# Kernel tuning notes

Measured on AMD Instinct MI355X. Metric: run time of the kernel, lower is better.

Reference implementation:

```python
import math
import jax, jax.numpy as jnp
import numpy as np

S, B, IN, D, H, L, F, WIN = 500, 32, 256, 512, 8, 2, 2048, 100


def setup_inputs() -> dict:
    key = jax.random.key(0)
    ks = jax.random.split(key, 20)
    s = 0.02
    inp = {
        "x": jax.random.normal(ks[0], (S, B, IN), dtype=jnp.float32),
        "W_emb": jax.random.normal(ks[1], (IN, D), dtype=jnp.float32) * s,
        "b_emb": jnp.zeros((D,), jnp.float32),
        "Wq": jax.random.normal(ks[2], (L, D, D), dtype=jnp.float32) * s,
        "bq": jnp.zeros((L, D), jnp.float32),
        "Wk": jax.random.normal(ks[3], (L, D, D), dtype=jnp.float32) * s,
        "bk": jnp.zeros((L, D), jnp.float32),
        "Wv": jax.random.normal(ks[4], (L, D, D), dtype=jnp.float32) * s,
        "bv": jnp.zeros((L, D), jnp.float32),
        "Wo": jax.random.normal(ks[5], (L, D, D), dtype=jnp.float32) * s,
        "bo": jnp.zeros((L, D), jnp.float32),
        "ln1_s": jnp.ones((L, D), jnp.float32),
        "ln1_b": jnp.zeros((L, D), jnp.float32),
        "W1": jax.random.normal(ks[6], (L, D, F), dtype=jnp.float32) * s,
        "b1": jnp.zeros((L, F), jnp.float32),
        "W2": jax.random.normal(ks[7], (L, F, D), dtype=jnp.float32) * s,
        "b2": jnp.zeros((L, D), jnp.float32),
        "ln2_s": jnp.ones((L, D), jnp.float32),
        "ln2_b": jnp.zeros((L, D), jnp.float32),
    }
    return inp


def _pos_encoding(seq_len, d_model, dtype):
    pos = jnp.arange(seq_len, dtype=dtype)[:, None]
    div = jnp.exp(jnp.arange(0, d_model, 2, dtype=dtype) * (-math.log(10000.0) / d_model))
    ang = pos * div  # [S, D/2]
    # interleave sin/cos -> pe[:,0::2]=sin, pe[:,1::2]=cos
    return jnp.stack([jnp.sin(ang), jnp.cos(ang)], axis=-1).reshape(seq_len, d_model)


def _layernorm(y, scale, bias, eps=1e-5):
    m = y.mean(-1, keepdims=True)
    v = ((y - m) ** 2).mean(-1, keepdims=True)
    return (y - m) / jnp.sqrt(v + eps) * scale + bias


def reference(x, W_emb, b_emb, Wq, bq, Wk, bk, Wv, bv, Wo, bo,
              ln1_s, ln1_b, W1, b1, W2, b2, ln2_s, ln2_b):
    seq_len, batch, _ = x.shape
    d_model = W_emb.shape[1]
    n_layers = Wq.shape[0]
    hd = d_model // H

    # embedding + positional encoding (dropout is identity in eval mode)
    h = x @ W_emb + b_emb + _pos_encoding(seq_len, d_model, x.dtype)[:, None, :]

    idx = jnp.arange(seq_len)
    diff = idx[:, None] - idx[None, :]
    amask = jnp.where((diff >= 0) & (diff < WIN), 0.0, -jnp.inf).astype(x.dtype)

    for l in range(n_layers):
        # multi-head self-attention (post-norm encoder layer)
        q = (h @ Wq[l] + bq[l]).reshape(seq_len, batch, H, hd)
        k = (h @ Wk[l] + bk[l]).reshape(seq_len, batch, H, hd)
        v = (h @ Wv[l] + bv[l]).reshape(seq_len, batch, H, hd)
        scores = jnp.einsum('ibhd,jbhd->bhij', q, k) / math.sqrt(hd) + amask
        attn = jax.nn.softmax(scores, axis=-1)
        o = jnp.einsum('bhij,jbhd->ibhd', attn, v).reshape(seq_len, batch, d_model)
        h = _layernorm(h + o @ Wo[l] + bo[l], ln1_s[l], ln1_b[l])
        # feed-forward (relu)
        ff = jax.nn.relu(h @ W1[l] + b1[l]) @ W2[l] + b2[l]
        h = _layernorm(h + ff, ln2_s[l], ln2_b[l])
    return h
```

## Files before the change

### kernel.cpp

```cpp
#include <hip/hip_runtime.h>
#include <stdint.h>

#define SEQ   500
#define BATCH 32
#define DIN   256
#define DM    512
#define NH    8
#define NL    2
#define DF    2048
#define WINSZ 100
#define HD    64
#define ROWS  (SEQ*BATCH)
#define MPAD  16128

typedef __bf16 bf16x8 __attribute__((ext_vector_type(8)));
typedef float  f32x4  __attribute__((ext_vector_type(4)));

__device__ __forceinline__ unsigned short bfbits(float f) {
    unsigned int u = __builtin_bit_cast(unsigned int, f);
    u = u + 0x7fffu + ((u >> 16) & 1u);
    return (unsigned short)(u >> 16);
}
__device__ __forceinline__ unsigned int pack2(float a, float b) {
    return (unsigned int)bfbits(a) | ((unsigned int)bfbits(b) << 16);
}
__device__ __forceinline__ float blo(unsigned int u) { return __builtin_bit_cast(float, u << 16); }
__device__ __forceinline__ float bhi(unsigned int u) { return __builtin_bit_cast(float, u & 0xffff0000u); }

__device__ __forceinline__ void async16(void* lds, const void* g) {
    __builtin_amdgcn_global_load_lds((__attribute__((address_space(1))) void*)(void*)g,
                                     (__attribute__((address_space(3))) void*)(void*)lds,
                                     16, 0, 0);
}

__global__ __launch_bounds__(256) void tcast_k(const float* __restrict__ src,
                                               unsigned short* __restrict__ dst,
                                               int R, int C) {
    __shared__ float t[32][33];
    int c0 = blockIdx.x * 32, r0 = blockIdx.y * 32;
    int tx = threadIdx.x, ty = threadIdx.y;
#pragma unroll
    for (int k = 0; k < 32; k += 8)
        t[ty + k][tx] = src[(size_t)(r0 + ty + k) * C + c0 + tx];
    __syncthreads();
#pragma unroll
    for (int k = 0; k < 32; k += 8)
        dst[(size_t)(c0 + ty + k) * R + r0 + tx] = bfbits(t[tx][ty + k]);
}

__global__ __launch_bounds__(256) void prep_k(const float* __restrict__ bq,
                                              const float* __restrict__ bk,
                                              const float* __restrict__ bv,
                                              float* __restrict__ bias_qkv,
                                              float* __restrict__ pe) {
    int tid = blockIdx.x * 256 + threadIdx.x;
    if (tid < SEQ * DM) {
        int s = tid >> 9, c = tid & 511;
        int p = c >> 1;
        float div = expf(-(float)(2 * p) * (9.210340371976184f / 512.0f));
        float ang = (float)s * div;
        pe[tid] = (c & 1) ? cosf(ang) : sinf(ang);
    }
    if (tid < NL * 3 * DM) {
        int l = tid / (3 * DM), r = tid % (3 * DM);
        float v = (r < DM) ? bq[l * DM + r]
                : (r < 2 * DM) ? bk[l * DM + r - DM]
                               : bv[l * DM + r - 2 * DM];
        bias_qkv[tid] = v;
    }
}

__global__ __launch_bounds__(256) void xcast_k(const float* __restrict__ x,
                                               unsigned short* __restrict__ xb, int n) {
    int i = (blockIdx.x * 256 + threadIdx.x) * 4;
    if (i < n) {
        float4 v = *(const float4*)&x[i];
        uint2 o; o.x = pack2(v.x, v.y); o.y = pack2(v.z, v.w);
        *(uint2*)&xb[i] = o;
    }
}

template <int MODE>
__global__ __launch_bounds__(256) void gemm_k(const unsigned short* __restrict__ A,
                                              const unsigned short* __restrict__ Wt,
                                              const float* __restrict__ bias,
                                              float* __restrict__ outF,
                                              unsigned short* __restrict__ outB,
                                              const float* __restrict__ pe,
                                              int M, int N, int K) {
    __shared__ unsigned short As[128 * 32];
    __shared__ unsigned short Bs[128 * 32];
    const int tid = threadIdx.x;
    const int lane = tid & 63, wid = tid >> 6;
    const int wr = wid >> 1, wc = wid & 1;
    const int m0 = blockIdx.x * 128, n0 = blockIdx.y * 128;
    const int lr = lane & 15, kg = (lane >> 4) * 8;

    f32x4 acc[4][4] = {};

    for (int k0 = 0; k0 < K; k0 += 32) {
#pragma unroll
        for (int r = 0; r < 2; ++r) {
            int chunk = r * 256 + tid;
            int row = chunk >> 2;
            int kc  = (chunk & 3) << 3;
            async16(&As[chunk * 8], A  + (size_t)(m0 + row) * K + k0 + kc);
            async16(&Bs[chunk * 8], Wt + (size_t)(n0 + row) * K + k0 + kc);
        }
        __syncthreads();
        bf16x8 af[4], bf[4];
#pragma unroll
        for (int f = 0; f < 4; ++f) {
            af[f] = *(const bf16x8*)&As[(wr * 64 + f * 16 + lr) * 32 + kg];
            bf[f] = *(const bf16x8*)&Bs[(wc * 64 + f * 16 + lr) * 32 + kg];
        }
#pragma unroll
        for (int i = 0; i < 4; ++i)
#pragma unroll
            for (int j = 0; j < 4; ++j)
                acc[i][j] = __builtin_amdgcn_mfma_f32_16x16x32_bf16(af[i], bf[j], acc[i][j], 0, 0, 0);
        __syncthreads();
    }

#pragma unroll
    for (int i = 0; i < 4; ++i) {
#pragma unroll
        for (int j = 0; j < 4; ++j) {
            int col = n0 + wc * 64 + j * 16 + lr;
            float bv = bias[col];
#pragma unroll
            for (int v = 0; v < 4; ++v) {
                int row = m0 + wr * 64 + i * 16 + (lane >> 4) * 4 + v;
                float val = acc[i][j][v] + bv;
                size_t idx = (size_t)row * N + col;
                if (MODE == 0) {
                    outF[idx] = val;
                } else if (MODE == 1) {
                    outB[idx] = bfbits(val);
                } else if (MODE == 2) {
                    outB[idx] = bfbits(fmaxf(val, 0.f));
                } else {
                    float t = val + pe[(size_t)(row >> 5) * DM + col];
                    outF[idx] = t;
                    outB[idx] = bfbits(t);
                }
            }
        }
    }
}

template <int BM, int BN, int MODE>
__global__ __launch_bounds__((BM == 256 ? 512 : 256), 2)
void gemm2_k(const unsigned short* __restrict__ A,
             const unsigned short* __restrict__ Wt,
             const float* __restrict__ bias,
             unsigned short* __restrict__ outB,
             int Mt, int Nt, int K, int N) {
    constexpr int NTH = (BM == 256) ? 512 : 256;
    constexpr int NWC = BN / 64;
    constexpr int NWR = (NTH / 64) / NWC;
    constexpr int MI  = BM / (NWR * 16);
    constexpr int MIH = (MI > 4) ? MI / 2 : MI;
    constexpr int JSH = (BN == 256) ? 6 : 5;

    __shared__ unsigned short LA[4][BM * 32];
    __shared__ unsigned short LB[4][BN * 32];

    const int tid = threadIdx.x, lane = tid & 63, wid = tid >> 6;
    const int wr = wid / NWC, wc = wid % NWC;
    const int lr = lane & 15, grp = lane >> 4;

    int lin = blockIdx.x;
    int base_m = (lin / (8 * Nt)) * 8;
    int Gc = min(8, Mt - base_m);
    int rem = lin - base_m * Nt;
    int mt = base_m + rem % Gc, nt = rem / Gc;
    const int m0 = mt * BM, n0 = nt * BN;

    const int NKT = K >> 5;

    auto stageA = [&](int kt, int part) {
        int slot = kt & 3, k0 = kt << 5;
        int g = part * NTH + tid;
        int row = g >> 2, c = g & 3;
        int src = c ^ ((row >> 1) & 3);
        async16(&LA[slot][g * 8], A + (size_t)(m0 + row) * K + k0 + src * 8);
    };
    auto stageB = [&](int kt, int part) {
        int slot = kt & 3, k0 = kt << 5;
        int g = part * NTH + tid;
        int pos = g >> 2, cs = g & 3;
        int j   = pos >> JSH;
        int wcc = (pos >> 4) & (NWC - 1);
        int lrr = pos & 15;
        int rb  = wcc * 64 + lrr * 4 + j;
        int c   = cs ^ ((rb >> 3) & 3);
        async16(&LB[slot][g * 8], Wt + (size_t)(n0 + rb) * K + k0 + c * 8);
    };

    f32x4 acc[MI][4] = {};

#pragma unroll
    for (int t = 0; t < 3; ++t) {
        stageA(t, 0); stageA(t, 1); stageB(t, 0); stageB(t, 1);
    }

    for (int kt = 0; kt < NKT; ++kt) {
        const int slot = kt & 3;
        const bool pf = (kt + 3 < NKT);
        if (kt + 2 < NKT)      asm volatile("s_waitcnt vmcnt(8)" ::: "memory");
        else if (kt + 1 < NKT) asm volatile("s_waitcnt vmcnt(4)" ::: "memory");
        else                   asm volatile("s_waitcnt vmcnt(0)" ::: "memory");
        __builtin_amdgcn_s_barrier();
        __builtin_amdgcn_sched_barrier(0);

        const int bxor = grp ^ ((lr >> 1) & 3);
        bf16x8 af[MI], bf[4];

#pragma unroll
        for (int i = 0; i < MIH; ++i) {
            int ra = wr * (MI * 16) + i * 16 + lr;
            af[i] = *(const bf16x8*)&LA[slot][ra * 32 + ((grp ^ ((ra >> 1) & 3)) << 3)];
        }
#pragma unroll
        for (int j = 0; j < 2; ++j) {
            int pos = j * (16 * NWC) + wc * 16 + lr;
            bf[j] = *(const bf16x8*)&LB[slot][(pos * 4 + bxor) * 8];
        }
        if (pf) { stageA(kt + 3, 0); if (MI == 4) stageA(kt + 3, 1); }
        __builtin_amdgcn_s_setprio(1);
#pragma unroll
        for (int i = 0; i < MIH; ++i)
#pragma unroll
            for (int j = 0; j < 2; ++j)
                acc[i][j] = __builtin_amdgcn_mfma_f32_16x16x32_bf16(af[i], bf[j], acc[i][j], 0, 0, 0);
        __builtin_amdgcn_s_setprio(0);
        __builtin_amdgcn_s_barrier();
        __builtin_amdgcn_sched_barrier(0);

#pragma unroll
        for (int j = 2; j < 4; ++j) {
            int pos = j * (16 * NWC) + wc * 16 + lr;
            bf[j] = *(const bf16x8*)&LB[slot][(pos * 4 + bxor) * 8];
        }
        if (pf) { if (MI == 4) { stageB(kt + 3, 0); stageB(kt + 3, 1); } else stageA(kt + 3, 1); }
        __builtin_amdgcn_s_setprio(1);
#pragma unroll
        for (int i = 0; i < MIH; ++i)
#pragma unroll
            for (int j = 2; j < 4; ++j)
                acc[i][j] = __builtin_amdgcn_mfma_f32_16x16x32_bf16(af[i], bf[j], acc[i][j], 0, 0, 0);
        __builtin_amdgcn_s_setprio(0);
        __builtin_amdgcn_s_barrier();
        __builtin_amdgcn_sched_barrier(0);

        if constexpr (MI > 4) {
#pragma unroll
            for (int i = MIH; i < MI; ++i) {
                int ra = wr * (MI * 16) + i * 16 + lr;
                af[i] = *(const bf16x8*)&LA[slot][ra * 32 + ((grp ^ ((ra >> 1) & 3)) << 3)];
            }
            if (pf) stageB(kt + 3, 0);
            __builtin_amdgcn_s_setprio(1);
#pragma unroll
            for (int i = MIH; i < MI; ++i)
#pragma unroll
                for (int j = 0; j < 2; ++j)
                    acc[i][j] = __builtin_amdgcn_mfma_f32_16x16x32_bf16(af[i], bf[j], acc[i][j], 0, 0, 0);
            __builtin_amdgcn_s_setprio(0);
            __builtin_amdgcn_s_barrier();
            __builtin_amdgcn_sched_barrier(0);

            if (pf) stageB(kt + 3, 1);
            __builtin_amdgcn_s_setprio(1);
#pragma unroll
            for (int i = MIH; i < MI; ++i)
#pragma unroll
                for (int j = 2; j < 4; ++j)
                    acc[i][j] = __builtin_amdgcn_mfma_f32_16x16x32_bf16(af[i], bf[j], acc[i][j], 0, 0, 0);
            __builtin_amdgcn_s_setprio(0);
            __builtin_amdgcn_s_barrier();
            __builtin_amdgcn_sched_barrier(0);
        }
    }

    const int colb = n0 + wc * 64 + lr * 4;
    float4 bv4 = *(const float4*)&bias[colb];
#pragma unroll
    for (int i = 0; i < MI; ++i) {
#pragma unroll
        for (int v = 0; v < 4; ++v) {
            int row = m0 + wr * (MI * 16) + i * 16 + grp * 4 + v;
            float f0 = acc[i][0][v] + bv4.x;
            float f1 = acc[i][1][v] + bv4.y;
            float f2 = acc[i][2][v] + bv4.z;
            float f3 = acc[i][3][v] + bv4.w;
            if (MODE == 2) {
                f0 = fmaxf(f0, 0.f); f1 = fmaxf(f1, 0.f);
                f2 = fmaxf(f2, 0.f); f3 = fmaxf(f3, 0.f);
            }
            uint2 wv; wv.x = pack2(f0, f1); wv.y = pack2(f2, f3);
            *(uint2*)&outB[(size_t)row * N + colb] = wv;
        }
    }
}

__global__ __launch_bounds__(256) void vtrans_k(const unsigned short* __restrict__ qkv,
                                                unsigned short* __restrict__ vT) {
    __shared__ unsigned short t[32][72];
    const int s0 = blockIdx.x * 32;
    const int bh = blockIdx.y;
    const int b = bh >> 3, h = bh & 7;
    const int tid = threadIdx.x;
    {
        int sl = tid >> 3;
        int c  = tid & 7;
        int s  = s0 + sl;
        uint4 val = {0, 0, 0, 0};
        if (s < SEQ)
            val = *(const uint4*)&qkv[(size_t)(s * BATCH + b) * (3 * DM) + 2 * DM + h * HD + c * 8];
        *(uint4*)&t[sl][c * 8] = val;
    }
    __syncthreads();
    {
        int d  = tid >> 2;
        int s8 = (tid & 3) * 8;
        unsigned short v[8];
#pragma unroll
        for (int j = 0; j < 8; ++j) v[j] = t[s8 + j][d];
        *(uint4*)&vT[(size_t)(bh * 64 + d) * 512 + s0 + s8] = *(uint4*)v;
    }
}

#define QBLK  64
#define NIB   8
#define KTIL  11
#define KSTR  72
#define VSTR  200
#define PSTR  200

__global__ __launch_bounds__(256, 3) void attn_k(const unsigned short* __restrict__ qkv,
                                                 const unsigned short* __restrict__ vT,
                                                 unsigned short* __restrict__ ob) {
    __shared__ unsigned short KV[12800];
    __shared__ unsigned short Pl[64 * PSTR];

    const int ib = blockIdx.x & (NIB - 1), bh = blockIdx.x >> 3;
    const int b = bh >> 3, h = bh & 7;
    const int i0 = ib * QBLK;
    const int jbase = max(0, i0 - (WINSZ - 1));
    const int jend  = min(SEQ - 1, i0 + QBLK - 1);
    const int nkeys = jend - jbase + 1;
    const int NT  = (nkeys + 15) >> 4;
    const int NKS = (nkeys + 31) >> 5;
    const int tid = threadIdx.x, lane = tid & 63, w = tid >> 6;
    const int q15 = lane & 15, grp = lane >> 4;

#pragma unroll
    for (int it = 0; it < 6; ++it) {
        int g = it * 256 + tid;
        if (g < 1408) {
            int row = g >> 3, c = g & 7;
            uint4 val = {0, 0, 0, 0};
            if (row < nkeys)
                val = *(const uint4*)&qkv[(size_t)((jbase + row) * BATCH + b) * (3 * DM)
                                          + DM + h * HD + c * 8];
            *(uint4*)&KV[row * KSTR + c * 8] = val;
        }
    }
#pragma unroll
    for (int it = 0; it < 7; ++it) {
        int g = it * 256 + tid;
        if (g < 1600) { uint4 z = {0, 0, 0, 0}; *(uint4*)&Pl[g * 8] = z; }
    }
    uint4 vreg[6];
#pragma unroll
    for (int it = 0; it < 6; ++it) {
        int g = it * 256 + tid;
        int r = g / 24, c = g - r * 24;
        uint4 val = {0, 0, 0, 0};
        if (c * 8 < nkeys && jbase + c * 8 + 8 <= 512)
            val = *(const uint4*)&vT[(size_t)(bh * 64 + r) * 512 + jbase + c * 8];
        vreg[it] = val;
    }
    bf16x8 qav, qbv;
    {
        int iq = min(i0 + w * 16 + q15, SEQ - 1);
        size_t qrow = (size_t)(iq * BATCH + b) * (3 * DM) + h * HD;
        uint4 a = *(const uint4*)&qkv[qrow + grp * 8];
        uint4 c = *(const uint4*)&qkv[qrow + 32 + grp * 8];
        qav = __builtin_bit_cast(bf16x8, a);
        qbv = __builtin_bit_cast(bf16x8, c);
    }
    __syncthreads();

    const int i = i0 + w * 16 + q15;
    float sc[KTIL][4];
#pragma unroll
    for (int t = 0; t < KTIL; ++t) {
        if (t >= NT) continue;
        f32x4 acc = {};
        int row = t * 16 + q15;
        bf16x8 kf0 = *(const bf16x8*)&KV[row * KSTR + grp * 8];
        acc = __builtin_amdgcn_mfma_f32_16x16x32_bf16(kf0, qav, acc, 0, 0, 0);
        bf16x8 kf1 = *(const bf16x8*)&KV[row * KSTR + 32 + grp * 8];
        acc = __builtin_amdgcn_mfma_f32_16x16x32_bf16(kf1, qbv, acc, 0, 0, 0);
#pragma unroll
        for (int v = 0; v < 4; ++v) {
            int key = jbase + t * 16 + grp * 4 + v;
            bool valid = (key <= i) && (key > i - WINSZ);
            sc[t][v] = valid ? acc[v] * 0.125f : -1e30f;
        }
    }
    float m = -1e30f;
#pragma unroll
    for (int t = 0; t < KTIL; ++t) {
        if (t >= NT) continue;
#pragma unroll
        for (int v = 0; v < 4; ++v) m = fmaxf(m, sc[t][v]);
    }
    m = fmaxf(m, __shfl_xor(m, 16));
    m = fmaxf(m, __shfl_xor(m, 32));
    float sum = 0.f;
#pragma unroll
    for (int t = 0; t < KTIL; ++t) {
        if (t >= NT) continue;
#pragma unroll
        for (int v = 0; v < 4; ++v) {
            float p = __expf(sc[t][v] - m);
            sc[t][v] = p;
            sum += p;
        }
    }
    sum += __shfl_xor(sum, 16);
    sum += __shfl_xor(sum, 32);

    __syncthreads();

#pragma unroll
    for (int it = 0; it < 6; ++it) {
        int g = it * 256 + tid;
        int r = g / 24, c = g - r * 24;
        *(uint4*)&KV[r * VSTR + c * 8] = vreg[it];
    }
#pragma unroll
    for (int t = 0; t < KTIL; ++t) {
        if (t >= NT) continue;
        uint2 pk;
        pk.x = pack2(sc[t][0], sc[t][1]);
        pk.y = pack2(sc[t][2], sc[t][3]);
        *(uint2*)&Pl[(w * 16 + q15) * PSTR + t * 16 + grp * 4] = pk;
    }
    __syncthreads();

    f32x4 oacc[4] = {};
#pragma unroll
    for (int ks = 0; ks < 6; ++ks) {
        if (ks >= NKS) continue;
        bf16x8 pf = *(const bf16x8*)&Pl[(w * 16 + q15) * PSTR + ks * 32 + grp * 8];
#pragma unroll
        for (int dt = 0; dt < 4; ++dt) {
            bf16x8 vf = *(const bf16x8*)&KV[(dt * 16 + q15) * VSTR + ks * 32 + grp * 8];
            oacc[dt] = __builtin_amdgcn_mfma_f32_16x16x32_bf16(pf, vf, oacc[dt], 0, 0, 0);
        }
    }

#pragma unroll
    for (int v = 0; v < 4; ++v) {
        float rsv = 1.0f / __shfl(sum, grp * 4 + v);
        int irow = i0 + w * 16 + grp * 4 + v;
        if (irow < SEQ) {
            size_t base = (size_t)(irow * BATCH + b) * DM + h * HD + q15;
#pragma unroll
            for (int dt = 0; dt < 4; ++dt)
                ob[base + dt * 16] = bfbits(oacc[dt][v] * rsv);
        }
    }
}

__global__ __launch_bounds__(256) void ln_k(const float* __restrict__ hin,
                                            const unsigned short* __restrict__ yin,
                                            const float* __restrict__ sc,
                                            const float* __restrict__ bi,
                                            float* __restrict__ hout,
                                            unsigned short* __restrict__ hb) {
    int row = blockIdx.x * 4 + (threadIdx.x >> 6);
    int lane = threadIdx.x & 63;
    size_t base = (size_t)row * DM + lane * 8;
    float4 a0 = *(const float4*)&hin[base], a1 = *(const float4*)&hin[base + 4];
    uint4 yw = *(const uint4*)&yin[base];
    float x[8] = {a0.x + blo(yw.x), a0.y + bhi(yw.x), a0.z + blo(yw.y), a0.w + bhi(yw.y),
                  a1.x + blo(yw.z), a1.y + bhi(yw.z), a1.z + blo(yw.w), a1.w + bhi(yw.w)};
    float s = 0.f;
#pragma unroll
    for (int k = 0; k < 8; ++k) s += x[k];
#pragma unroll
    for (int off = 32; off; off >>= 1) s += __shfl_xor(s, off);
    float mean = s * (1.f / DM);
    float q = 0.f;
#pragma unroll
    for (int k = 0; k < 8; ++k) { float d = x[k] - mean; q = fmaf(d, d, q); }
#pragma unroll
    for (int off = 32; off; off >>= 1) q += __shfl_xor(q, off);
    float rstd = rsqrtf(q * (1.f / DM) + 1e-5f);
    float4 s0 = *(const float4*)&sc[lane * 8], s1 = *(const float4*)&sc[lane * 8 + 4];
    float4 b0 = *(const float4*)&bi[lane * 8], b1 = *(const float4*)&bi[lane * 8 + 4];
    float o[8];
    o[0] = (x[0] - mean) * rstd * s0.x + b0.x;  o[1] = (x[1] - mean) * rstd * s0.y + b0.y;
    o[2] = (x[2] - mean) * rstd * s0.z + b0.z;  o[3] = (x[3] - mean) * rstd * s0.w + b0.w;
    o[4] = (x[4] - mean) * rstd * s1.x + b1.x;  o[5] = (x[5] - mean) * rstd * s1.y + b1.y;
    o[6] = (x[6] - mean) * rstd * s1.z + b1.z;  o[7] = (x[7] - mean) * rstd * s1.w + b1.w;
    float4 w0 = {o[0], o[1], o[2], o[3]}, w1 = {o[4], o[5], o[6], o[7]};
    *(float4*)&hout[base] = w0;
    *(float4*)&hout[base + 4] = w1;
    uint4 pk = {pack2(o[0], o[1]), pack2(o[2], o[3]), pack2(o[4], o[5]), pack2(o[6], o[7])};
    *(uint4*)&hb[base] = pk;
}

extern "C" void kernel_launch(void* const* d_in, const int* in_sizes, int n_in,
                              void* d_out, int out_size, void* d_ws, size_t ws_size,
                              hipStream_t stream) {
    const float* x     = (const float*)d_in[0];
    const float* Wemb  = (const float*)d_in[1];
    const float* bemb  = (const float*)d_in[2];
    const float* Wq    = (const float*)d_in[3];
    const float* bq    = (const float*)d_in[4];
    const float* Wk    = (const float*)d_in[5];
    const float* bk    = (const float*)d_in[6];
    const float* Wv    = (const float*)d_in[7];
    const float* bv    = (const float*)d_in[8];
    const float* Wo    = (const float*)d_in[9];
    const float* bo    = (const float*)d_in[10];
    const float* ln1s  = (const float*)d_in[11];
    const float* ln1b  = (const float*)d_in[12];
    const float* W1    = (const float*)d_in[13];
    const float* b1    = (const float*)d_in[14];
    const float* W2    = (const float*)d_in[15];
    const float* b2    = (const float*)d_in[16];
    const float* ln2s  = (const float*)d_in[17];
    const float* ln2b  = (const float*)d_in[18];

    char* p = (char*)d_ws;
    auto carve = [&](size_t bytes) { char* r = p; p += (bytes + 255) & ~(size_t)255; return r; };

    unsigned short* wt_emb = (unsigned short*)carve((size_t)DM * DIN * 2);
    unsigned short* wt_qkv = (unsigned short*)carve((size_t)NL * 3 * DM * DM * 2);
    unsigned short* wt_o   = (unsigned short*)carve((size_t)NL * DM * DM * 2);
    unsigned short* wt_1   = (unsigned short*)carve((size_t)NL * DF * DM * 2);
    unsigned short* wt_2   = (unsigned short*)carve((size_t)NL * DM * DF * 2);
    float*          biasq  = (float*)carve((size_t)NL * 3 * DM * 4);
    float*          pe     = (float*)carve((size_t)SEQ * DM * 4);
    unsigned short* xb     = (unsigned short*)carve((size_t)ROWS * DIN * 2);
    float*          h      = (float*)carve((size_t)ROWS * DM * 4);
    unsigned short* hb     = (unsigned short*)carve((size_t)MPAD * DM * 2);
    unsigned short* ob     = (unsigned short*)carve((size_t)MPAD * DM * 2);
    unsigned short* t0b    = (unsigned short*)carve((size_t)MPAD * DM * 2);
    unsigned short* vT     = (unsigned short*)carve((size_t)BATCH * NH * 64 * 512 * 2 + 1024);
    unsigned short* qkv    = (unsigned short*)carve((size_t)MPAD * DF * 2);
    unsigned short* f1     = qkv;

    dim3 blk256(256);

    tcast_k<<<dim3(DM / 32, DIN / 32), dim3(32, 8), 0, stream>>>(Wemb, wt_emb, DIN, DM);
    for (int l = 0; l < NL; ++l) {
        tcast_k<<<dim3(DM / 32, DM / 32), dim3(32, 8), 0, stream>>>(Wq + (size_t)l * DM * DM, wt_qkv + (size_t)l * 3 * DM * DM, DM, DM);
        tcast_k<<<dim3(DM / 32, DM / 32), dim3(32, 8), 0, stream>>>(Wk + (size_t)l * DM * DM, wt_qkv + (size_t)l * 3 * DM * DM + (size_t)DM * DM, DM, DM);
        tcast_k<<<dim3(DM / 32, DM / 32), dim3(32, 8), 0, stream>>>(Wv + (size_t)l * DM * DM, wt_qkv + (size_t)l * 3 * DM * DM + (size_t)2 * DM * DM, DM, DM);
        tcast_k<<<dim3(DM / 32, DM / 32), dim3(32, 8), 0, stream>>>(Wo + (size_t)l * DM * DM, wt_o + (size_t)l * DM * DM, DM, DM);
        tcast_k<<<dim3(DF / 32, DM / 32), dim3(32, 8), 0, stream>>>(W1 + (size_t)l * DM * DF, wt_1 + (size_t)l * DF * DM, DM, DF);
        tcast_k<<<dim3(DM / 32, DF / 32), dim3(32, 8), 0, stream>>>(W2 + (size_t)l * DF * DM, wt_2 + (size_t)l * DM * DF, DF, DM);
    }
    prep_k<<<dim3((SEQ * DM + 255) / 256), blk256, 0, stream>>>(bq, bk, bv, biasq, pe);
    xcast_k<<<dim3(ROWS * DIN / 4 / 256), blk256, 0, stream>>>(x, xb, ROWS * DIN);

    gemm_k<3><<<dim3(ROWS / 128, DM / 128), blk256, 0, stream>>>(xb, wt_emb, bemb, h, hb, pe, ROWS, DM, DIN);

    const int Mt256 = MPAD / 256;
    const int Mt128 = MPAD / 128;
    for (int l = 0; l < NL; ++l) {
        gemm2_k<256, 256, 1><<<dim3(Mt256 * 6), dim3(512), 0, stream>>>(
            hb, wt_qkv + (size_t)l * 3 * DM * DM, biasq + (size_t)l * 3 * DM,
            qkv, Mt256, 6, DM, 3 * DM);
        vtrans_k<<<dim3(16, BATCH * NH), blk256, 0, stream>>>(qkv, vT);
        attn_k<<<dim3(BATCH * NH * NIB), blk256, 0, stream>>>(qkv, vT, ob);
        gemm2_k<128, 128, 1><<<dim3(Mt128 * 4), blk256, 0, stream>>>(
            ob, wt_o + (size_t)l * DM * DM, bo + (size_t)l * DM,
            t0b, Mt128, 4, DM, DM);
        ln_k<<<dim3(ROWS / 4), blk256, 0, stream>>>(h, t0b, ln1s + (size_t)l * DM, ln1b + (size_t)l * DM, h, hb);
        gemm2_k<256, 256, 2><<<dim3(Mt256 * 8), dim3(512), 0, stream>>>(
            hb, wt_1 + (size_t)l * DF * DM, b1 + (size_t)l * DF,
            f1, Mt256, 8, DM, DF);
        gemm2_k<128, 128, 1><<<dim3(Mt128 * 4), blk256, 0, stream>>>(
            f1, wt_2 + (size_t)l * DM * DF, b2 + (size_t)l * DM,
            t0b, Mt128, 4, DF, DM);
        float* hdst = (l == NL - 1) ? (float*)d_out : h;
        ln_k<<<dim3(ROWS / 4), blk256, 0, stream>>>(h, t0b, ln2s + (size_t)l * DM, ln2b + (size_t)l * DM, hdst, hb);
    }
}
```

Baseline: 482.1 us.

## Keep residual stream in bf16 only and use 3-slot pipeline for 128-tile GEMMs

Drops the fp32 copy of the hidden state. The embedding GEMM and the layernorm kernels now read and write only the bf16 residual buffer, and only the final layernorm writes fp32 output. This cuts memory traffic in the layernorm and embedding kernels, at the cost of extra rounding in the residual path. It also gives the 128x128 GEMM variant 3 LDS slots with prefetch distance 2 instead of 4, lowering its shared-memory footprint, which may raise occupancy.

```diff
diff --git a/kernel.cpp b/kernel.cpp
--- a/kernel.cpp
+++ b/kernel.cpp
@@ -84,7 +84,6 @@
 __global__ __launch_bounds__(256) void gemm_k(const unsigned short* __restrict__ A,
                                               const unsigned short* __restrict__ Wt,
                                               const float* __restrict__ bias,
-                                              float* __restrict__ outF,
                                               unsigned short* __restrict__ outB,
                                               const float* __restrict__ pe,
                                               int M, int N, int K) {
@@ -133,15 +132,12 @@
                 int row = m0 + wr * 64 + i * 16 + (lane >> 4) * 4 + v;
                 float val = acc[i][j][v] + bv;
                 size_t idx = (size_t)row * N + col;
-                if (MODE == 0) {
-                    outF[idx] = val;
-                } else if (MODE == 1) {
+                if (MODE == 1) {
                     outB[idx] = bfbits(val);
                 } else if (MODE == 2) {
                     outB[idx] = bfbits(fmaxf(val, 0.f));
                 } else {
                     float t = val + pe[(size_t)(row >> 5) * DM + col];
-                    outF[idx] = t;
                     outB[idx] = bfbits(t);
                 }
             }
@@ -157,14 +153,16 @@
              unsigned short* __restrict__ outB,
              int Mt, int Nt, int K, int N) {
     constexpr int NTH = (BM == 256) ? 512 : 256;
+    constexpr int SLOTS = (BM == 256) ? 4 : 3;
+    constexpr int PD  = SLOTS - 1;
     constexpr int NWC = BN / 64;
     constexpr int NWR = (NTH / 64) / NWC;
     constexpr int MI  = BM / (NWR * 16);
     constexpr int MIH = (MI > 4) ? MI / 2 : MI;
     constexpr int JSH = (BN == 256) ? 6 : 5;
 
-    __shared__ unsigned short LA[4][BM * 32];
-    __shared__ unsigned short LB[4][BN * 32];
+    __shared__ unsigned short LA[SLOTS][BM * 32];
+    __shared__ unsigned short LB[SLOTS][BN * 32];
 
     const int tid = threadIdx.x, lane = tid & 63, wid = tid >> 6;
     const int wr = wid / NWC, wc = wid % NWC;
@@ -180,14 +178,14 @@
     const int NKT = K >> 5;
 
     auto stageA = [&](int kt, int part) {
-        int slot = kt & 3, k0 = kt << 5;
+        int slot = kt % SLOTS, k0 = kt << 5;
         int g = part * NTH + tid;
         int row = g >> 2, c = g & 3;
         int src = c ^ ((row >> 1) & 3);
         async16(&LA[slot][g * 8], A + (size_t)(m0 + row) * K + k0 + src * 8);
     };
     auto stageB = [&](int kt, int part) {
-        int slot = kt & 3, k0 = kt << 5;
+        int slot = kt % SLOTS, k0 = kt << 5;
         int g = part * NTH + tid;
         int pos = g >> 2, cs = g & 3;
         int j   = pos >> JSH;
@@ -201,16 +199,21 @@
     f32x4 acc[MI][4] = {};
 
 #pragma unroll
-    for (int t = 0; t < 3; ++t) {
+    for (int t = 0; t < PD; ++t) {
         stageA(t, 0); stageA(t, 1); stageB(t, 0); stageB(t, 1);
     }
 
     for (int kt = 0; kt < NKT; ++kt) {
-        const int slot = kt & 3;
-        const bool pf = (kt + 3 < NKT);
-        if (kt + 2 < NKT)      asm volatile("s_waitcnt vmcnt(8)" ::: "memory");
-        else if (kt + 1 < NKT) asm volatile("s_waitcnt vmcnt(4)" ::: "memory");
-        else                   asm volatile("s_waitcnt vmcnt(0)" ::: "memory");
+        const int slot = kt % SLOTS;
+        const bool pf = (kt + PD < NKT);
+        if constexpr (PD == 3) {
+            if (kt + 2 < NKT)      asm volatile("s_waitcnt vmcnt(8)" ::: "memory");
+            else if (kt + 1 < NKT) asm volatile("s_waitcnt vmcnt(4)" ::: "memory");
+            else                   asm volatile("s_waitcnt vmcnt(0)" ::: "memory");
+        } else {
+            if (kt + 1 < NKT)      asm volatile("s_waitcnt vmcnt(4)" ::: "memory");
+            else                   asm volatile("s_waitcnt vmcnt(0)" ::: "memory");
+        }
         __builtin_amdgcn_s_barrier();
         __builtin_amdgcn_sched_barrier(0);
 
@@ -227,7 +230,7 @@
             int pos = j * (16 * NWC) + wc * 16 + lr;
             bf[j] = *(const bf16x8*)&LB[slot][(pos * 4 + bxor) * 8];
         }
-        if (pf) { stageA(kt + 3, 0); if (MI == 4) stageA(kt + 3, 1); }
+        if (pf) { stageA(kt + PD, 0); if (MI == 4) stageA(kt + PD, 1); }
         __builtin_amdgcn_s_setprio(1);
 #pragma unroll
         for (int i = 0; i < MIH; ++i)
@@ -243,7 +246,7 @@
             int pos = j * (16 * NWC) + wc * 16 + lr;
             bf[j] = *(const bf16x8*)&LB[slot][(pos * 4 + bxor) * 8];
         }
-        if (pf) { if (MI == 4) { stageB(kt + 3, 0); stageB(kt + 3, 1); } else stageA(kt + 3, 1); }
+        if (pf) { if (MI == 4) { stageB(kt + PD, 0); stageB(kt + PD, 1); } else stageA(kt + PD, 1); }
         __builtin_amdgcn_s_setprio(1);
 #pragma unroll
         for (int i = 0; i < MIH; ++i)
@@ -260,7 +263,7 @@
                 int ra = wr * (MI * 16) + i * 16 + lr;
                 af[i] = *(const bf16x8*)&LA[slot][ra * 32 + ((grp ^ ((ra >> 1) & 3)) << 3)];
             }
-            if (pf) stageB(kt + 3, 0);
+            if (pf) stageB(kt + PD, 0);
             __builtin_amdgcn_s_setprio(1);
 #pragma unroll
             for (int i = MIH; i < MI; ++i)
@@ -271,7 +274,7 @@
             __builtin_amdgcn_s_barrier();
             __builtin_amdgcn_sched_barrier(0);
 
-            if (pf) stageB(kt + 3, 1);
+            if (pf) stageB(kt + PD, 1);
             __builtin_amdgcn_s_setprio(1);
 #pragma unroll
             for (int i = MIH; i < MI; ++i)
@@ -478,19 +481,22 @@
     }
 }
 
-__global__ __launch_bounds__(256) void ln_k(const float* __restrict__ hin,
+template <int FOUT>
+__global__ __launch_bounds__(256) void ln_k(const unsigned short* __restrict__ hin,
                                             const unsigned short* __restrict__ yin,
                                             const float* __restrict__ sc,
                                             const float* __restrict__ bi,
-                                            float* __restrict__ hout,
-                                            unsigned short* __restrict__ hb) {
+                                            unsigned short* __restrict__ hb,
+                                            float* __restrict__ fout) {
     int row = blockIdx.x * 4 + (threadIdx.x >> 6);
     int lane = threadIdx.x & 63;
     size_t base = (size_t)row * DM + lane * 8;
-    float4 a0 = *(const float4*)&hin[base], a1 = *(const float4*)&hin[base + 4];
+    uint4 hw = *(const uint4*)&hin[base];
     uint4 yw = *(const uint4*)&yin[base];
-    float x[8] = {a0.x + blo(yw.x), a0.y + bhi(yw.x), a0.z + blo(yw.y), a0.w + bhi(yw.y),
-                  a1.x + blo(yw.z), a1.y + bhi(yw.z), a1.z + blo(yw.w), a1.w + bhi(yw.w)};
+    float x[8] = {blo(hw.x) + blo(yw.x), bhi(hw.x) + bhi(yw.x),
+                  blo(hw.y) + blo(yw.y), bhi(hw.y) + bhi(yw.y),
+                  blo(hw.z) + blo(yw.z), bhi(hw.z) + bhi(yw.z),
+                  blo(hw.w) + blo(yw.w), bhi(hw.w) + bhi(yw.w)};
     float s = 0.f;
 #pragma unroll
     for (int k = 0; k < 8; ++k) s += x[k];
@@ -510,11 +516,14 @@
     o[2] = (x[2] - mean) * rstd * s0.z + b0.z;  o[3] = (x[3] - mean) * rstd * s0.w + b0.w;
     o[4] = (x[4] - mean) * rstd * s1.x + b1.x;  o[5] = (x[5] - mean) * rstd * s1.y + b1.y;
     o[6] = (x[6] - mean) * rstd * s1.z + b1.z;  o[7] = (x[7] - mean) * rstd * s1.w + b1.w;
-    float4 w0 = {o[0], o[1], o[2], o[3]}, w1 = {o[4], o[5], o[6], o[7]};
-    *(float4*)&hout[base] = w0;
-    *(float4*)&hout[base + 4] = w1;
-    uint4 pk = {pack2(o[0], o[1]), pack2(o[2], o[3]), pack2(o[4], o[5]), pack2(o[6], o[7])};
-    *(uint4*)&hb[base] = pk;
+    if (FOUT) {
+        float4 w0 = {o[0], o[1], o[2], o[3]}, w1 = {o[4], o[5], o[6], o[7]};
+        *(float4*)&fout[base] = w0;
+        *(float4*)&fout[base + 4] = w1;
+    } else {
+        uint4 pk = {pack2(o[0], o[1]), pack2(o[2], o[3]), pack2(o[4], o[5]), pack2(o[6], o[7])};
+        *(uint4*)&hb[base] = pk;
+    }
 }
 
 extern "C" void kernel_launch(void* const* d_in, const int* in_sizes, int n_in,
@@ -551,8 +560,7 @@
     float*          biasq  = (float*)carve((size_t)NL * 3 * DM * 4);
     float*          pe     = (float*)carve((size_t)SEQ * DM * 4);
     unsigned short* xb     = (unsigned short*)carve((size_t)ROWS * DIN * 2);
-    float*          h      = (float*)carve((size_t)ROWS * DM * 4);
-    unsigned short* hb     = (unsigned short*)carve((size_t)MPAD * DM * 2);
+    unsigned short* h      = (unsigned short*)carve((size_t)MPAD * DM * 2);
     unsigned short* ob     = (unsigned short*)carve((size_t)MPAD * DM * 2);
     unsigned short* t0b    = (unsigned short*)carve((size_t)MPAD * DM * 2);
     unsigned short* vT     = (unsigned short*)carve((size_t)BATCH * NH * 64 * 512 * 2 + 1024);
@@ -573,27 +581,29 @@
     prep_k<<<dim3((SEQ * DM + 255) / 256), blk256, 0, stream>>>(bq, bk, bv, biasq, pe);
     xcast_k<<<dim3(ROWS * DIN / 4 / 256), blk256, 0, stream>>>(x, xb, ROWS * DIN);
 
-    gemm_k<3><<<dim3(ROWS / 128, DM / 128), blk256, 0, stream>>>(xb, wt_emb, bemb, h, hb, pe, ROWS, DM, DIN);
+    gemm_k<3><<<dim3(ROWS / 128, DM / 128), blk256, 0, stream>>>(xb, wt_emb, bemb, h, pe, ROWS, DM, DIN);
 
     const int Mt256 = MPAD / 256;
     const int Mt128 = MPAD / 128;
     for (int l = 0; l < NL; ++l) {
         gemm2_k<256, 256, 1><<<dim3(Mt256 * 6), dim3(512), 0, stream>>>(
-            hb, wt_qkv + (size_t)l * 3 * DM * DM, biasq + (size_t)l * 3 * DM,
+            h, wt_qkv + (size_t)l * 3 * DM * DM, biasq + (size_t)l * 3 * DM,
             qkv, Mt256, 6, DM, 3 * DM);
         vtrans_k<<<dim3(16, BATCH * NH), blk256, 0, stream>>>(qkv, vT);
         attn_k<<<dim3(BATCH * NH * NIB), blk256, 0, stream>>>(qkv, vT, ob);
         gemm2_k<128, 128, 1><<<dim3(Mt128 * 4), blk256, 0, stream>>>(
             ob, wt_o + (size_t)l * DM * DM, bo + (size_t)l * DM,
             t0b, Mt128, 4, DM, DM);
-        ln_k<<<dim3(ROWS / 4), blk256, 0, stream>>>(h, t0b, ln1s + (size_t)l * DM, ln1b + (size_t)l * DM, h, hb);
+        ln_k<0><<<dim3(ROWS / 4), blk256, 0, stream>>>(h, t0b, ln1s + (size_t)l * DM, ln1b + (size_t)l * DM, h, nullptr);
         gemm2_k<256, 256, 2><<<dim3(Mt256 * 8), dim3(512), 0, stream>>>(
-            hb, wt_1 + (size_t)l * DF * DM, b1 + (size_t)l * DF,
+            h, wt_1 + (size_t)l * DF * DM, b1 + (size_t)l * DF,
             f1, Mt256, 8, DM, DF);
         gemm2_k<128, 128, 1><<<dim3(Mt128 * 4), blk256, 0, stream>>>(
             f1, wt_2 + (size_t)l * DM * DF, b2 + (size_t)l * DM,
             t0b, Mt128, 4, DF, DM);
-        float* hdst = (l == NL - 1) ? (float*)d_out : h;
-        ln_k<<<dim3(ROWS / 4), blk256, 0, stream>>>(h, t0b, ln2s + (size_t)l * DM, ln2b + (size_t)l * DM, hdst, hb);
-    }
-}
+        if (l == NL - 1)
+            ln_k<1><<<dim3(ROWS / 4), blk256, 0, stream>>>(h, t0b, ln2s + (size_t)l * DM, ln2b + (size_t)l * DM, nullptr, (float*)d_out);
+        else
+            ln_k<0><<<dim3(ROWS / 4), blk256, 0, stream>>>(h, t0b, ln2s + (size_t)l * DM, ln2b + (size_t)l * DM, h, nullptr);
+    }
+}
```

Result: faster. 444.0 us (-7.9%).
